# Kernel optimization log

Hardware: AMD Instinct MI355X
Metric: run time of the kernel (lower is better)

## Reference

```python
import jax, jax.numpy as jnp
import numpy as np

N, E, EL = 100000, 1600000, 200000
DIN, DH, DOUT = 128, 128, 64


def _glorot(k, fi, fo):
    return jax.random.normal(k, (fi, fo), jnp.float32) * jax.lax.rsqrt(jnp.float32(fi))


def setup_inputs() -> dict:
    key = jax.random.key(0)
    ks = jax.random.split(key, 8)
    x = jax.random.normal(ks[0], (N, DIN), jnp.float32)
    edge_index = jax.random.randint(ks[1], (2, E), 0, N)
    edge_label_index = jax.random.randint(ks[2], (2, EL), 0, N)
    return {
        "x": x,
        "W1": _glorot(ks[3], DIN, DH), "b1": jnp.zeros((DH,), jnp.float32),
        "W2": _glorot(ks[4], DH, DH), "b2": jnp.zeros((DH,), jnp.float32),
        "W3": _glorot(ks[5], DH, DOUT), "b3": jnp.zeros((DOUT,), jnp.float32),
        "edge_index": edge_index,
        "edge_label_index": edge_label_index,
    }


def gcn_conv(x, W, b, src, dst, norm, n):
    # PyG GCNConv: h = x @ W; out[dst] += norm * h[src]; out += b
    h = x @ W
    msg = h[src] * norm[:, None]                       # [E+N, d]
    out = jax.ops.segment_sum(msg, dst, num_segments=n)
    return out + b


def reference(x, W1, b1, W2, b2, W3, b3, edge_index, edge_label_index):
    n = x.shape[0]
    loop = jnp.arange(n, dtype=edge_index.dtype)
    src = jnp.concatenate([edge_index[0], loop])       # self-loops appended
    dst = jnp.concatenate([edge_index[1], loop])
    # symmetric normalization: deg from dst (col), norm = d^-1/2[src] * d^-1/2[dst]
    deg = jax.ops.segment_sum(jnp.ones(dst.shape[0], x.dtype), dst, num_segments=n)
    dis = jnp.where(deg > 0, jax.lax.rsqrt(jnp.maximum(deg, 1.0)), 0.0)
    norm = dis[src] * dis[dst]

    z = jax.nn.relu(gcn_conv(x, W1, b1, src, dst, norm, n))
    z = jax.nn.relu(gcn_conv(z, W2, b2, src, dst, norm, n))
    z = gcn_conv(z, W3, b3, src, dst, norm, n)

    # decode
    hidden = z[edge_label_index[0]] * z[edge_label_index[1]]   # [EL, DOUT]
    logits = hidden.sum(axis=-1)                               # [EL]
    nrm = jnp.maximum(jnp.linalg.norm(hidden, axis=1, keepdims=True), 1e-12)
    hidden_n = hidden / nrm                                    # F.normalize(dim=1)
    return (hidden_n, logits)
```

## Files before the change

### kernel.cpp

```cpp
#include <hip/hip_runtime.h>
#include <hip/hip_bf16.h>

#define DIN 128
#define DH  128
#define DOUT 64

#define BSHIFT 9
#define BNODES 512
#define BCAP   12288
#define CHUNK  4096

typedef __attribute__((ext_vector_type(8))) short short8;
typedef __attribute__((ext_vector_type(4))) float f32x4;

static __device__ __forceinline__ unsigned short f2bf(float f) {
    unsigned int u = __float_as_uint(f);
    u += 0x7FFFu + ((u >> 16) & 1u);
    return (unsigned short)(u >> 16);
}
static __device__ __forceinline__ float bflo(unsigned int p) {
    return __uint_as_float(p << 16);
}
static __device__ __forceinline__ float bfhi(unsigned int p) {
    return __uint_as_float(p & 0xFFFF0000u);
}

__global__ __launch_bounds__(256) void prep_w_kernel(const float* __restrict__ W1,
                                                     const float* __restrict__ W2,
                                                     const float* __restrict__ W3,
                                                     unsigned short* __restrict__ Wt1,
                                                     unsigned short* __restrict__ Wt2,
                                                     unsigned short* __restrict__ Wt3,
                                                     int* __restrict__ gcur) {
    int i = blockIdx.x * 256 + threadIdx.x;
    if (blockIdx.x == 0) gcur[threadIdx.x] = 0;
    if (i < 128 * 128) {
        int n = i >> 7, k = i & 127;
        Wt1[n * 128 + k] = f2bf(W1[k * 128 + n]);
        Wt2[n * 128 + k] = f2bf(W2[k * 128 + n]);
        if (n < 64) Wt3[n * 128 + k] = f2bf(W3[k * 64 + n]);
    }
}

__global__ __launch_bounds__(256) void bin_scatter_kernel(const int* __restrict__ ei, int E,
                                                          int* __restrict__ gcur,
                                                          int* __restrict__ pairs) {
    __shared__ int hist[256];
    __shared__ int base[256];
    int t = threadIdx.x;
    hist[t] = 0;
    __syncthreads();
    int e0 = blockIdx.x * CHUNK;
    int srcs[16], dsts[16], rk[16];
    #pragma unroll
    for (int j = 0; j < 16; j++) {
        int e = e0 + j * 256 + t;
        if (e < E) {
            srcs[j] = ei[e];
            dsts[j] = ei[E + e];
            rk[j] = atomicAdd(&hist[dsts[j] >> BSHIFT], 1);
        } else {
            rk[j] = -1;
        }
    }
    __syncthreads();
    base[t] = (hist[t] > 0) ? atomicAdd(&gcur[t], hist[t]) : 0;
    __syncthreads();
    #pragma unroll
    for (int j = 0; j < 16; j++) {
        if (rk[j] >= 0) {
            int b = dsts[j] >> BSHIFT;
            int dl = dsts[j] & (BNODES - 1);
            pairs[(size_t)b * BCAP + base[b] + rk[j]] = (dl << 17) | srcs[j];
        }
    }
}

__global__ __launch_bounds__(256) void bucket_deg_kernel(const int* __restrict__ pairs,
                                                         const int* __restrict__ gcur,
                                                         int* __restrict__ deg, int n) {
    __shared__ int cnt_l[BNODES];
    int t = threadIdx.x, b = blockIdx.x;
    cnt_l[t] = 0; cnt_l[t + 256] = 0;
    __syncthreads();
    int cnt = gcur[b];
    const int* p = pairs + (size_t)b * BCAP;
    for (int i = t; i < cnt; i += 256) {
        int pk = p[i];
        atomicAdd(&cnt_l[pk >> 17], 1);
    }
    __syncthreads();
    int node = (b << BSHIFT) + t;
    if (node < n) deg[node] = cnt_l[t] + 1;
    node += 256;
    if (node < n) deg[node] = cnt_l[t + 256] + 1;
}

__global__ __launch_bounds__(256) void scan_block_sums(const int* __restrict__ deg,
                                                       int* __restrict__ bsum, int n) {
    __shared__ int s[256];
    int t = threadIdx.x, base = blockIdx.x * 1024;
    int v = 0;
    #pragma unroll
    for (int j = 0; j < 4; j++) {
        int idx = base + t * 4 + j;
        if (idx < n) v += deg[idx];
    }
    s[t] = v; __syncthreads();
    for (int off = 128; off > 0; off >>= 1) {
        if (t < off) s[t] += s[t + off];
        __syncthreads();
    }
    if (t == 0) bsum[blockIdx.x] = s[0];
}

__global__ __launch_bounds__(256) void scan_bsum_kernel(int* __restrict__ bsum, int nb) {
    __shared__ int s[256];
    int t = threadIdx.x;
    s[t] = (t < nb) ? bsum[t] : 0; __syncthreads();
    for (int off = 1; off < 256; off <<= 1) {
        int v = (t >= off) ? s[t - off] : 0;
        __syncthreads();
        s[t] += v;
        __syncthreads();
    }
    if (t < nb) bsum[t] = (t > 0) ? s[t - 1] : 0;
}

__global__ __launch_bounds__(256) void scan_final_kernel(const int* __restrict__ deg,
                                                         const int* __restrict__ bsum_ex,
                                                         int* __restrict__ row_start,
                                                         float* __restrict__ dis,
                                                         int* __restrict__ csr_src, int n) {
    __shared__ int s[256];
    int t = threadIdx.x, base = blockIdx.x * 1024;
    int d[4]; int local = 0;
    #pragma unroll
    for (int j = 0; j < 4; j++) {
        int idx = base + t * 4 + j;
        d[j] = (idx < n) ? deg[idx] : 0;
        local += d[j];
    }
    s[t] = local; __syncthreads();
    for (int off = 1; off < 256; off <<= 1) {
        int v = (t >= off) ? s[t - off] : 0;
        __syncthreads();
        s[t] += v;
        __syncthreads();
    }
    int ex = ((t > 0) ? s[t - 1] : 0) + bsum_ex[blockIdx.x];
    #pragma unroll
    for (int j = 0; j < 4; j++) {
        int idx = base + t * 4 + j;
        if (idx < n) {
            row_start[idx] = ex;
            float di = rsqrtf((float)d[j]);
            dis[idx] = di;
            csr_src[ex] = idx;
            if (idx == n - 1) row_start[n] = ex + d[j];
            ex += d[j];
        }
    }
}

__global__ __launch_bounds__(256) void bucket_fill_kernel(const int* __restrict__ pairs,
                                                          const int* __restrict__ gcur,
                                                          const int* __restrict__ row_start,
                                                          int* __restrict__ csr_src, int n) {
    __shared__ int cur[BNODES];
    int t = threadIdx.x, b = blockIdx.x;
    int node = (b << BSHIFT) + t;
    cur[t] = (node < n) ? row_start[node] + 1 : 0;
    int node2 = node + 256;
    cur[t + 256] = (node2 < n) ? row_start[node2] + 1 : 0;
    __syncthreads();
    int cnt = gcur[b];
    const int* p = pairs + (size_t)b * BCAP;
    for (int i = t; i < cnt; i += 256) {
        int pk = p[i];
        int pos = atomicAdd(&cur[pk >> 17], 1);
        csr_src[pos] = pk & 0x1FFFF;
    }
}

template <int NOUT, bool AFP32>
__global__ __launch_bounds__(256) void gemm_bf16_kernel(const void* __restrict__ Av,
                                                        const unsigned short* __restrict__ Wt,
                                                        const float* __restrict__ dis,
                                                        unsigned short* __restrict__ H, int M) {
    int wave = (blockIdx.x * 256 + threadIdx.x) >> 6;
    int lane = threadIdx.x & 63;
    int m0 = wave << 4;
    if (m0 >= M) return;
    int m = lane & 15, q = lane >> 4;
    constexpr int NT = NOUT / 16;
    f32x4 acc[NT];
    #pragma unroll
    for (int t = 0; t < NT; t++) acc[t] = (f32x4){0.f, 0.f, 0.f, 0.f};
    const short8* Arow = (const short8*)((const unsigned short*)Av + (size_t)(m0 + m) * 128);
    const float*  Arow32 = (const float*)Av + (size_t)(m0 + m) * 128;
    #pragma unroll
    for (int kk = 0; kk < 4; kk++) {
        short8 a;
        if (AFP32) {
            float4 u = *(const float4*)(Arow32 + kk * 32 + q * 8);
            float4 v = *(const float4*)(Arow32 + kk * 32 + q * 8 + 4);
            a[0] = (short)f2bf(u.x); a[1] = (short)f2bf(u.y);
            a[2] = (short)f2bf(u.z); a[3] = (short)f2bf(u.w);
            a[4] = (short)f2bf(v.x); a[5] = (short)f2bf(v.y);
            a[6] = (short)f2bf(v.z); a[7] = (short)f2bf(v.w);
        } else {
            a = Arow[kk * 4 + q];
        }
        #pragma unroll
        for (int t = 0; t < NT; t++) {
            const short8* Bp = (const short8*)(Wt + (size_t)(t * 16 + m) * 128);
            short8 b = Bp[kk * 4 + q];
            acc[t] = __builtin_amdgcn_mfma_f32_16x16x32_bf16(a, b, acc[t], 0, 0, 0);
        }
    }
    float ds[4];
    #pragma unroll
    for (int r = 0; r < 4; r++) ds[r] = dis[m0 + q * 4 + r];
    #pragma unroll
    for (int t = 0; t < NT; t++)
        #pragma unroll
        for (int r = 0; r < 4; r++)
            H[(size_t)(m0 + q * 4 + r) * NOUT + t * 16 + m] = f2bf(acc[t][r] * ds[r]);
}

template <int EPL, bool RELU, bool OUTBF>
__global__ __launch_bounds__(256) void aggregate_kernel(const unsigned short* __restrict__ H,
                                                        const int* __restrict__ row_start,
                                                        const int* __restrict__ csr_src,
                                                        const float* __restrict__ dis,
                                                        const float* __restrict__ bias,
                                                        void* __restrict__ out, int n) {
    constexpr int F = EPL * 16;
    int row = (blockIdx.x * 256 + threadIdx.x) >> 4;
    int gl  = threadIdx.x & 15;
    if (row >= n) return;
    int c = gl * EPL;
    float acc[EPL];
    #pragma unroll
    for (int i = 0; i < EPL; i++) acc[i] = 0.f;
    int p0 = row_start[row], p1 = row_start[row + 1];
    int p = p0;
    for (; p + 8 <= p1; p += 8) {
        int e[8];
        #pragma unroll
        for (int u = 0; u < 8; u++) e[u] = csr_src[p + u];
        if (EPL == 8) {
            uint4 h[8];
            #pragma unroll
            for (int u = 0; u < 8; u++) h[u] = *(const uint4*)(H + (size_t)e[u] * F + c);
            #pragma unroll
            for (int u = 0; u < 8; u++) {
                acc[0] += bflo(h[u].x); acc[1] += bfhi(h[u].x);
                acc[2] += bflo(h[u].y); acc[3] += bfhi(h[u].y);
                acc[4] += bflo(h[u].z); acc[5] += bfhi(h[u].z);
                acc[6] += bflo(h[u].w); acc[7] += bfhi(h[u].w);
            }
        } else {
            uint2 h[8];
            #pragma unroll
            for (int u = 0; u < 8; u++) h[u] = *(const uint2*)(H + (size_t)e[u] * F + c);
            #pragma unroll
            for (int u = 0; u < 8; u++) {
                acc[0] += bflo(h[u].x); acc[1] += bfhi(h[u].x);
                acc[2] += bflo(h[u].y); acc[3] += bfhi(h[u].y);
            }
        }
    }
    for (; p + 4 <= p1; p += 4) {
        int e0 = csr_src[p],     e1 = csr_src[p + 1];
        int e2 = csr_src[p + 2], e3 = csr_src[p + 3];
        if (EPL == 8) {
            uint4 h0 = *(const uint4*)(H + (size_t)e0 * F + c);
            uint4 h1 = *(const uint4*)(H + (size_t)e1 * F + c);
            uint4 h2 = *(const uint4*)(H + (size_t)e2 * F + c);
            uint4 h3 = *(const uint4*)(H + (size_t)e3 * F + c);
            acc[0] += bflo(h0.x) + bflo(h1.x) + bflo(h2.x) + bflo(h3.x);
            acc[1] += bfhi(h0.x) + bfhi(h1.x) + bfhi(h2.x) + bfhi(h3.x);
            acc[2] += bflo(h0.y) + bflo(h1.y) + bflo(h2.y) + bflo(h3.y);
            acc[3] += bfhi(h0.y) + bfhi(h1.y) + bfhi(h2.y) + bfhi(h3.y);
            acc[4] += bflo(h0.z) + bflo(h1.z) + bflo(h2.z) + bflo(h3.z);
            acc[5] += bfhi(h0.z) + bfhi(h1.z) + bfhi(h2.z) + bfhi(h3.z);
            acc[6] += bflo(h0.w) + bflo(h1.w) + bflo(h2.w) + bflo(h3.w);
            acc[7] += bfhi(h0.w) + bfhi(h1.w) + bfhi(h2.w) + bfhi(h3.w);
        } else {
            uint2 h0 = *(const uint2*)(H + (size_t)e0 * F + c);
            uint2 h1 = *(const uint2*)(H + (size_t)e1 * F + c);
            uint2 h2 = *(const uint2*)(H + (size_t)e2 * F + c);
            uint2 h3 = *(const uint2*)(H + (size_t)e3 * F + c);
            acc[0] += bflo(h0.x) + bflo(h1.x) + bflo(h2.x) + bflo(h3.x);
            acc[1] += bfhi(h0.x) + bfhi(h1.x) + bfhi(h2.x) + bfhi(h3.x);
            acc[2] += bflo(h0.y) + bflo(h1.y) + bflo(h2.y) + bflo(h3.y);
            acc[3] += bfhi(h0.y) + bfhi(h1.y) + bfhi(h2.y) + bfhi(h3.y);
        }
    }
    for (; p < p1; p++) {
        int e = csr_src[p];
        if (EPL == 8) {
            uint4 h = *(const uint4*)(H + (size_t)e * F + c);
            acc[0] += bflo(h.x); acc[1] += bfhi(h.x);
            acc[2] += bflo(h.y); acc[3] += bfhi(h.y);
            acc[4] += bflo(h.z); acc[5] += bfhi(h.z);
            acc[6] += bflo(h.w); acc[7] += bfhi(h.w);
        } else {
            uint2 h = *(const uint2*)(H + (size_t)e * F + c);
            acc[0] += bflo(h.x); acc[1] += bfhi(h.x);
            acc[2] += bflo(h.y); acc[3] += bfhi(h.y);
        }
    }
    float dd = dis[row];
    #pragma unroll
    for (int i = 0; i < EPL; i++) {
        acc[i] = acc[i] * dd + bias[c + i];
        if (RELU) acc[i] = fmaxf(acc[i], 0.f);
    }
    if (OUTBF) {
        unsigned short* ob = (unsigned short*)out + (size_t)row * F + c;
        if (EPL == 8) {
            uint4 pk;
            pk.x = ((unsigned int)f2bf(acc[1]) << 16) | f2bf(acc[0]);
            pk.y = ((unsigned int)f2bf(acc[3]) << 16) | f2bf(acc[2]);
            pk.z = ((unsigned int)f2bf(acc[5]) << 16) | f2bf(acc[4]);
            pk.w = ((unsigned int)f2bf(acc[7]) << 16) | f2bf(acc[6]);
            *(uint4*)ob = pk;
        } else {
            uint2 pk;
            pk.x = ((unsigned int)f2bf(acc[1]) << 16) | f2bf(acc[0]);
            pk.y = ((unsigned int)f2bf(acc[3]) << 16) | f2bf(acc[2]);
            *(uint2*)ob = pk;
        }
    } else {
        float* of = (float*)out + (size_t)row * F + c;
        #pragma unroll
        for (int i = 0; i < EPL; i += 4) {
            *(float4*)(of + i) = make_float4(acc[i], acc[i + 1], acc[i + 2], acc[i + 3]);
        }
    }
}

__global__ __launch_bounds__(256) void decode_kernel(const float* __restrict__ Z,
                                                     const int* __restrict__ eli, int EL,
                                                     float* __restrict__ out_h,
                                                     float* __restrict__ out_l) {
    int g  = (blockIdx.x * 256 + threadIdx.x) >> 4;
    int gl = threadIdx.x & 15;
    int q0 = g * 2;
    if (q0 >= EL) return;
    int q1 = q0 + 1;
    bool has1 = q1 < EL;
    int a0 = eli[q0], b0 = eli[EL + q0];
    int a1 = has1 ? eli[q1] : a0;
    int b1 = has1 ? eli[EL + q1] : b0;
    float4 za0 = *(const float4*)(Z + (size_t)a0 * 64 + gl * 4);
    float4 zb0 = *(const float4*)(Z + (size_t)b0 * 64 + gl * 4);
    float4 za1 = *(const float4*)(Z + (size_t)a1 * 64 + gl * 4);
    float4 zb1 = *(const float4*)(Z + (size_t)b1 * 64 + gl * 4);

    float h00 = za0.x * zb0.x, h01 = za0.y * zb0.y, h02 = za0.z * zb0.z, h03 = za0.w * zb0.w;
    float h10 = za1.x * zb1.x, h11 = za1.y * zb1.y, h12 = za1.z * zb1.z, h13 = za1.w * zb1.w;
    float s0  = h00 + h01 + h02 + h03;
    float ss0 = h00 * h00 + h01 * h01 + h02 * h02 + h03 * h03;
    float s1  = h10 + h11 + h12 + h13;
    float ss1 = h10 * h10 + h11 * h11 + h12 * h12 + h13 * h13;
    #pragma unroll
    for (int off = 8; off > 0; off >>= 1) {
        s0  += __shfl_xor(s0, off, 64);
        ss0 += __shfl_xor(ss0, off, 64);
        s1  += __shfl_xor(s1, off, 64);
        ss1 += __shfl_xor(ss1, off, 64);
    }
    float inv0 = 1.0f / fmaxf(sqrtf(ss0), 1e-12f);
    *(float4*)(out_h + (size_t)q0 * 64 + gl * 4) =
        make_float4(h00 * inv0, h01 * inv0, h02 * inv0, h03 * inv0);
    if (gl == 0) out_l[q0] = s0;
    if (has1) {
        float inv1 = 1.0f / fmaxf(sqrtf(ss1), 1e-12f);
        *(float4*)(out_h + (size_t)q1 * 64 + gl * 4) =
            make_float4(h10 * inv1, h11 * inv1, h12 * inv1, h13 * inv1);
        if (gl == 0) out_l[q1] = s1;
    }
}

extern "C" void kernel_launch(void* const* d_in, const int* in_sizes, int n_in,
                              void* d_out, int out_size, void* d_ws, size_t ws_size,
                              hipStream_t stream) {
    const float* x  = (const float*)d_in[0];
    const float* W1 = (const float*)d_in[1];
    const float* b1 = (const float*)d_in[2];
    const float* W2 = (const float*)d_in[3];
    const float* b2 = (const float*)d_in[4];
    const float* W3 = (const float*)d_in[5];
    const float* b3 = (const float*)d_in[6];
    const int* edge_index = (const int*)d_in[7];
    const int* eli        = (const int*)d_in[8];

    const int N  = in_sizes[0] / DIN;
    const int E  = in_sizes[7] / 2;
    const int EL = in_sizes[8] / 2;
    const int NBUCK = (N + BNODES - 1) >> BSHIFT;

    char* w = (char*)d_ws;
    auto alloc = [&](size_t bytes) -> char* {
        char* p = w; w += (bytes + 255) & ~(size_t)255; return p;
    };
    unsigned short* bufA  = (unsigned short*)alloc((size_t)N * DH * 2);
    float*          Z3    = (float*)alloc((size_t)N * DOUT * 4);
    unsigned short* Xbf   = (unsigned short*)alloc((size_t)N * DH * 2);
    unsigned short* Wt1   = (unsigned short*)alloc(128 * 128 * 2);
    unsigned short* Wt2   = (unsigned short*)alloc(128 * 128 * 2);
    unsigned short* Wt3   = (unsigned short*)alloc(64 * 128 * 2);
    int*            deg   = (int*)alloc((size_t)N * 4);
    int*            row_start = (int*)alloc((size_t)(N + 1) * 4);
    float*          dis    = (float*)alloc((size_t)N * 4);
    int*            bsum   = (int*)alloc(1024);
    int*            gcur   = (int*)alloc(256 * 4);
    int*            csr_src = (int*)alloc((size_t)(E + N) * 4);
    int*            pairs  = (int*)alloc((size_t)NBUCK * BCAP * 4);

    float* out_h = (float*)d_out;
    float* out_l = out_h + (size_t)EL * DOUT;

    const int NB = (N + 1023) / 1024;

    prep_w_kernel<<<64, 256, 0, stream>>>(W1, W2, W3, Wt1, Wt2, Wt3, gcur);
    bin_scatter_kernel<<<(E + CHUNK - 1) / CHUNK, 256, 0, stream>>>(edge_index, E, gcur, pairs);
    bucket_deg_kernel<<<NBUCK, 256, 0, stream>>>(pairs, gcur, deg, N);
    scan_block_sums<<<NB, 256, 0, stream>>>(deg, bsum, N);
    scan_bsum_kernel<<<1, 256, 0, stream>>>(bsum, NB);
    scan_final_kernel<<<NB, 256, 0, stream>>>(deg, bsum, row_start, dis, csr_src, N);
    bucket_fill_kernel<<<NBUCK, 256, 0, stream>>>(pairs, gcur, row_start, csr_src, N);

    const int gemm_grid = ((N / 16) * 64 + 255) / 256;
    const int agg_grid  = (N * 16 + 255) / 256;

    gemm_bf16_kernel<128, true><<<gemm_grid, 256, 0, stream>>>(x, Wt1, dis, bufA, N);
    aggregate_kernel<8, true, true><<<agg_grid, 256, 0, stream>>>(bufA, row_start, csr_src, dis, b1, Xbf, N);
    gemm_bf16_kernel<128, false><<<gemm_grid, 256, 0, stream>>>(Xbf, Wt2, dis, bufA, N);
    aggregate_kernel<8, true, true><<<agg_grid, 256, 0, stream>>>(bufA, row_start, csr_src, dis, b2, Xbf, N);
    gemm_bf16_kernel<64, false><<<gemm_grid, 256, 0, stream>>>(Xbf, Wt3, dis, bufA, N);
    aggregate_kernel<4, false, false><<<agg_grid, 256, 0, stream>>>(bufA, row_start, csr_src, dis, b3, Z3, N);
    const int dec_groups = (EL + 1) / 2;
    decode_kernel<<<(dec_groups * 16 + 255) / 256, 256, 0, stream>>>(Z3, eli, EL, out_h, out_l);
}
```

Baseline: 437.5 us.

## Fuse aggregation with following layer GEMM via shared-memory tile

Adds a kernel that aggregates 16 destination rows of neighbor features, applies bias and ReLU, stores the bf16 result in shared memory, and immediately runs the next layer's MFMA GEMM on that tile. Layers 1→2 and 2→3 are now aggregate+GEMM fused, removing the round trip of the intermediate activation buffer and two kernel launches. The trade-off is that the GEMM weights are reloaded per 16-row block and gather latency can now stall the GEMM phase within the same block. The fused kernel also adds a __syncthreads between the two phases.

Measured after the change: 415.8 us. 5.0% less time.

```diff
diff --git a/kernel.cpp b/kernel.cpp
--- a/kernel.cpp
+++ b/kernel.cpp
@@ -227,6 +227,107 @@
         #pragma unroll
         for (int r = 0; r < 4; r++)
             H[(size_t)(m0 + q * 4 + r) * NOUT + t * 16 + m] = f2bf(acc[t][r] * ds[r]);
+}
+
+template <int NOUT>
+__global__ __launch_bounds__(256) void agg_gemm_kernel(const unsigned short* __restrict__ H,
+                                                       const int* __restrict__ row_start,
+                                                       const int* __restrict__ csr_src,
+                                                       const float* __restrict__ dis,
+                                                       const float* __restrict__ bias,
+                                                       const unsigned short* __restrict__ Wt,
+                                                       unsigned short* __restrict__ Hout,
+                                                       int n) {
+    __shared__ unsigned short X[16][128];
+    int t = threadIdx.x;
+    int g = t >> 4, gl = t & 15;
+    int row = blockIdx.x * 16 + g;
+    int c = gl * 8;
+    float acc[8];
+    #pragma unroll
+    for (int i = 0; i < 8; i++) acc[i] = 0.f;
+    if (row < n) {
+        int p0 = row_start[row], p1 = row_start[row + 1];
+        int p = p0;
+        for (; p + 8 <= p1; p += 8) {
+            int e[8];
+            #pragma unroll
+            for (int u = 0; u < 8; u++) e[u] = csr_src[p + u];
+            uint4 h[8];
+            #pragma unroll
+            for (int u = 0; u < 8; u++) h[u] = *(const uint4*)(H + (size_t)e[u] * 128 + c);
+            #pragma unroll
+            for (int u = 0; u < 8; u++) {
+                acc[0] += bflo(h[u].x); acc[1] += bfhi(h[u].x);
+                acc[2] += bflo(h[u].y); acc[3] += bfhi(h[u].y);
+                acc[4] += bflo(h[u].z); acc[5] += bfhi(h[u].z);
+                acc[6] += bflo(h[u].w); acc[7] += bfhi(h[u].w);
+            }
+        }
+        for (; p + 4 <= p1; p += 4) {
+            int e0 = csr_src[p],     e1 = csr_src[p + 1];
+            int e2 = csr_src[p + 2], e3 = csr_src[p + 3];
+            uint4 h0 = *(const uint4*)(H + (size_t)e0 * 128 + c);
+            uint4 h1 = *(const uint4*)(H + (size_t)e1 * 128 + c);
+            uint4 h2 = *(const uint4*)(H + (size_t)e2 * 128 + c);
+            uint4 h3 = *(const uint4*)(H + (size_t)e3 * 128 + c);
+            acc[0] += bflo(h0.x) + bflo(h1.x) + bflo(h2.x) + bflo(h3.x);
+            acc[1] += bfhi(h0.x) + bfhi(h1.x) + bfhi(h2.x) + bfhi(h3.x);
+            acc[2] += bflo(h0.y) + bflo(h1.y) + bflo(h2.y) + bflo(h3.y);
+            acc[3] += bfhi(h0.y) + bfhi(h1.y) + bfhi(h2.y) + bfhi(h3.y);
+            acc[4] += bflo(h0.z) + bflo(h1.z) + bflo(h2.z) + bflo(h3.z);
+            acc[5] += bfhi(h0.z) + bfhi(h1.z) + bfhi(h2.z) + bfhi(h3.z);
+            acc[6] += bflo(h0.w) + bflo(h1.w) + bflo(h2.w) + bflo(h3.w);
+            acc[7] += bfhi(h0.w) + bfhi(h1.w) + bfhi(h2.w) + bfhi(h3.w);
+        }
+        for (; p < p1; p++) {
+            int e = csr_src[p];
+            uint4 h = *(const uint4*)(H + (size_t)e * 128 + c);
+            acc[0] += bflo(h.x); acc[1] += bfhi(h.x);
+            acc[2] += bflo(h.y); acc[3] += bfhi(h.y);
+            acc[4] += bflo(h.z); acc[5] += bfhi(h.z);
+            acc[6] += bflo(h.w); acc[7] += bfhi(h.w);
+        }
+        float dd = dis[row];
+        #pragma unroll
+        for (int i = 0; i < 8; i++)
+            acc[i] = fmaxf(acc[i] * dd + bias[c + i], 0.f);
+    }
+    uint4 pk;
+    pk.x = ((unsigned int)f2bf(acc[1]) << 16) | f2bf(acc[0]);
+    pk.y = ((unsigned int)f2bf(acc[3]) << 16) | f2bf(acc[2]);
+    pk.z = ((unsigned int)f2bf(acc[5]) << 16) | f2bf(acc[4]);
+    pk.w = ((unsigned int)f2bf(acc[7]) << 16) | f2bf(acc[6]);
+    *(uint4*)&X[g][c] = pk;
+    __syncthreads();
+    int wv = t >> 6, lane = t & 63;
+    int m = lane & 15, q = lane >> 4;
+    constexpr int TPW = (NOUT / 16 + 3) / 4;
+    f32x4 gacc[TPW];
+    #pragma unroll
+    for (int tt = 0; tt < TPW; tt++) gacc[tt] = (f32x4){0.f, 0.f, 0.f, 0.f};
+    #pragma unroll
+    for (int kk = 0; kk < 4; kk++) {
+        short8 a = *(const short8*)&X[m][kk * 32 + q * 8];
+        #pragma unroll
+        for (int tt = 0; tt < TPW; tt++) {
+            int tile = wv * TPW + tt;
+            const short8* Bp = (const short8*)(Wt + (size_t)(tile * 16 + m) * 128);
+            short8 b = Bp[kk * 4 + q];
+            gacc[tt] = __builtin_amdgcn_mfma_f32_16x16x32_bf16(a, b, gacc[tt], 0, 0, 0);
+        }
+    }
+    int base = blockIdx.x * 16;
+    #pragma unroll
+    for (int r = 0; r < 4; r++) {
+        int rr = base + q * 4 + r;
+        if (rr < n) {
+            float ds = dis[rr];
+            #pragma unroll
+            for (int tt = 0; tt < TPW; tt++)
+                Hout[(size_t)rr * NOUT + (wv * TPW + tt) * 16 + m] = f2bf(gacc[tt][r] * ds);
+        }
+    }
 }
 
 template <int EPL, bool RELU, bool OUTBF>
@@ -409,8 +510,8 @@
         char* p = w; w += (bytes + 255) & ~(size_t)255; return p;
     };
     unsigned short* bufA  = (unsigned short*)alloc((size_t)N * DH * 2);
+    unsigned short* bufB  = (unsigned short*)alloc((size_t)N * DH * 2);
     float*          Z3    = (float*)alloc((size_t)N * DOUT * 4);
-    unsigned short* Xbf   = (unsigned short*)alloc((size_t)N * DH * 2);
     unsigned short* Wt1   = (unsigned short*)alloc(128 * 128 * 2);
     unsigned short* Wt2   = (unsigned short*)alloc(128 * 128 * 2);
     unsigned short* Wt3   = (unsigned short*)alloc(64 * 128 * 2);
@@ -436,13 +537,12 @@
     bucket_fill_kernel<<<NBUCK, 256, 0, stream>>>(pairs, gcur, row_start, csr_src, N);
 
     const int gemm_grid = ((N / 16) * 64 + 255) / 256;
+    const int fuse_grid = (N + 15) / 16;
     const int agg_grid  = (N * 16 + 255) / 256;
 
     gemm_bf16_kernel<128, true><<<gemm_grid, 256, 0, stream>>>(x, Wt1, dis, bufA, N);
-    aggregate_kernel<8, true, true><<<agg_grid, 256, 0, stream>>>(bufA, row_start, csr_src, dis, b1, Xbf, N);
-    gemm_bf16_kernel<128, false><<<gemm_grid, 256, 0, stream>>>(Xbf, Wt2, dis, bufA, N);
-    aggregate_kernel<8, true, true><<<agg_grid, 256, 0, stream>>>(bufA, row_start, csr_src, dis, b2, Xbf, N);
-    gemm_bf16_kernel<64, false><<<gemm_grid, 256, 0, stream>>>(Xbf, Wt3, dis, bufA, N);
+    agg_gemm_kernel<128><<<fuse_grid, 256, 0, stream>>>(bufA, row_start, csr_src, dis, b1, Wt2, bufB, N);
+    agg_gemm_kernel<64><<<fuse_grid, 256, 0, stream>>>(bufB, row_start, csr_src, dis, b2, Wt3, bufA, N);
     aggregate_kernel<4, false, false><<<agg_grid, 256, 0, stream>>>(bufA, row_start, csr_src, dis, b3, Z3, N);
     const int dec_groups = (EL + 1) / 2;
     decode_kernel<<<(dec_groups * 16 + 255) / 256, 256, 0, stream>>>(Z3, eli, EL, out_h, out_l);
```
